# Optimization experiments

Hardware: AMD Instinct MI355X
Metric: run time of the kernel (lower is better)

## Reference

```python
import jax, jax.numpy as jnp
import numpy as np

B = 32
SIZES = [5023, 1256, 314, 79]
NS = [s + 1 for s in SIZES]   # padded vertex counts per level: [5024,1257,315,80]
K = 9
ENC_C = [3, 64, 128, 256]
DEC_C = [256, 128, 64, 3]
LATENT = 256


def _feast(x, nbr, wm, bm, wc, bc, act):
    # x: [B,N,F]; nbr: [N,K] int32 (col 0 = self index)
    xn = jnp.transpose(x[:, nbr, :], (0, 1, 3, 2))          # [B,N,F,K]
    xr = xn - xn[..., :1]                                    # relative to self neighbor
    logits = jnp.einsum('bnfk,of->bnok', xr, wm) + bm[None, None, :, None]  # conv1d(F->K,1)
    perm = jax.nn.softmax(logits, axis=2)                    # softmax over out-channel dim (torch dim=1)
    agg = jnp.einsum('bnfk,bnko->bnfo', xn, perm)            # [B,N,F,K] batched matmul
    Bv, N, F, Kv = agg.shape
    y = act(agg.reshape(Bv, N, F * Kv) @ wc.T + bc)          # linear(F*K -> out)
    mask = jnp.ones((N, 1), y.dtype).at[-1, 0].set(0.0)      # zero out padding vertex
    return y * mask


def _pool(x, L):
    # x: [B,M,F]; L: [Mp,M] -> [B,Mp,F]  (dense form of torch.spmm pooling)
    return jnp.einsum('pm,bmf->bpf', L, x)


def _forward(x, nbrs, Ds, Us, enc_p, dec_p, fce_w, fce_b, fcd_w, fcd_b):
    elu = jax.nn.elu
    ident = lambda v: v
    for i in range(3):
        wm, bm, wc, bc = enc_p[i]
        x = _feast(x, nbrs[i], wm, bm, wc, bc, elu)
        x = _pool(x, Ds[i])
    z = x.reshape(B, -1) @ fce_w.T + fce_b                    # [B, latent]
    x = (z @ fcd_w.T + fcd_b).reshape(B, NS[3], DEC_C[0])
    dec_nbrs = [nbrs[2], nbrs[1], nbrs[0]]
    dec_Us = [Us[2], Us[1], Us[0]]
    acts = [elu, elu, ident]                                  # last dconv uses identity
    for i in range(3):
        x = _pool(x, dec_Us[i])
        wm, bm, wc, bc = dec_p[i]
        x = _feast(x, dec_nbrs[i], wm, bm, wc, bc, acts[i])
    return x


def setup_inputs() -> dict:
    key = jax.random.key(0)
    ks = iter(jax.random.split(key, 64))
    nrm = lambda sh, s=0.05: jax.random.normal(next(ks), sh, dtype=jnp.float32) * s
    inp = {}
    inp['x'] = jax.random.normal(next(ks), (B, NS[0], 3), dtype=jnp.float32)
    for i in range(3):
        n = NS[i]
        nb = jax.random.randint(next(ks), (n, K), 0, n)
        nb = nb.at[:, 0].set(jnp.arange(n))
        inp[f'nbr{i}'] = nb.astype(jnp.int32)
    for i in range(3):
        cols = jax.random.randint(next(ks), (NS[i + 1],), 0, NS[i])
        inp[f'D{i}'] = jax.nn.one_hot(cols, NS[i], dtype=jnp.float32)   # sparse-like pooling
        cols_u = jax.random.randint(next(ks), (NS[i],), 0, NS[i + 1])
        inp[f'U{i}'] = jax.nn.one_hot(cols_u, NS[i + 1], dtype=jnp.float32)
    for i in range(3):
        fi, fo = ENC_C[i], ENC_C[i + 1]
        inp[f'e{i}_wm'] = nrm((K, fi)); inp[f'e{i}_bm'] = jnp.zeros((K,), jnp.float32)
        inp[f'e{i}_wc'] = nrm((fo, fi * K)); inp[f'e{i}_bc'] = jnp.zeros((fo,), jnp.float32)
    inp['fce_w'] = nrm((LATENT, NS[3] * ENC_C[3])); inp['fce_b'] = jnp.zeros((LATENT,), jnp.float32)
    inp['fcd_w'] = nrm((NS[3] * DEC_C[0], LATENT)); inp['fcd_b'] = jnp.zeros((NS[3] * DEC_C[0],), jnp.float32)
    for i in range(3):
        fi, fo = DEC_C[i], DEC_C[i + 1]
        inp[f'd{i}_wm'] = nrm((K, fi)); inp[f'd{i}_bm'] = jnp.zeros((K,), jnp.float32)
        inp[f'd{i}_wc'] = nrm((fo, fi * K)); inp[f'd{i}_bc'] = jnp.zeros((fo,), jnp.float32)
    return inp


def reference(x, nbr0, nbr1, nbr2, D0, D1, D2, U0, U1, U2,
              e0_wm, e0_bm, e0_wc, e0_bc, e1_wm, e1_bm, e1_wc, e1_bc,
              e2_wm, e2_bm, e2_wc, e2_bc, fce_w, fce_b, fcd_w, fcd_b,
              d0_wm, d0_bm, d0_wc, d0_bc, d1_wm, d1_bm, d1_wc, d1_bc,
              d2_wm, d2_bm, d2_wc, d2_bc):
    nbrs = [nbr0, nbr1, nbr2]
    Ds = [D0, D1, D2]
    Us = [U0, U1, U2]
    enc_p = [(e0_wm, e0_bm, e0_wc, e0_bc), (e1_wm, e1_bm, e1_wc, e1_bc), (e2_wm, e2_bm, e2_wc, e2_bc)]
    dec_p = [(d0_wm, d0_bm, d0_wc, d0_bc), (d1_wm, d1_bm, d1_wc, d1_bc), (d2_wm, d2_bm, d2_wc, d2_bc)]
    return _forward(x, nbrs, Ds, Us, enc_p, dec_p, fce_w, fce_b, fcd_w, fcd_b)
```

## Files before the change

### kernel.cpp

```cpp
#include <hip/hip_runtime.h>
#include <cstddef>

#define KN 9
typedef unsigned short u16;
typedef unsigned int u32;
typedef __attribute__((ext_vector_type(8))) short short8;
typedef __attribute__((ext_vector_type(4))) float f32x4;

__device__ inline u16 f2b(float f) {
    union { float f; u32 u; } v; v.f = f;
    u32 r = v.u + 0x7FFFu + ((v.u >> 16) & 1u);
    return (u16)(r >> 16);
}
__device__ inline float b2f(u16 h) {
    union { u32 u; float f; } v; v.u = ((u32)h) << 16; return v.f;
}

__device__ inline int xcd_swz(int bid, int n) {
    int q = n >> 3, r = n & 7;
    int x = bid & 7, pos = bid >> 3;
    return (x < r ? x * (q + 1) : r * (q + 1) + (x - r) * q) + pos;
}

__global__ void extract_idx_all(
    const float* __restrict__ D0, const float* __restrict__ D1, const float* __restrict__ D2,
    const float* __restrict__ U0, const float* __restrict__ U1, const float* __restrict__ U2,
    int* __restrict__ iD0, int* __restrict__ iD1, int* __restrict__ iD2,
    int* __restrict__ iU0, int* __restrict__ iU1, int* __restrict__ iU2)
{
    int blk = blockIdx.x;
    const float* L; int M; int* out; int p;
    if      (blk < 1257) { L = D0; M = 5024; out = iD0; p = blk; }
    else if (blk < 1572) { L = D1; M = 1257; out = iD1; p = blk - 1257; }
    else if (blk < 1652) { L = D2; M = 315;  out = iD2; p = blk - 1572; }
    else if (blk < 6676) { L = U0; M = 1257; out = iU0; p = blk - 1652; }
    else if (blk < 7933) { L = U1; M = 315;  out = iU1; p = blk - 6676; }
    else                 { L = U2; M = 80;   out = iU2; p = blk - 7933; }
    const float* row = L + (size_t)p * M;
    for (int m = threadIdx.x; m < M; m += 256)
        if (row[m] > 0.5f) out[p] = m;
}

__global__ void zero_f32(float4* __restrict__ p, int n4)
{
    int t = blockIdx.x * 256 + threadIdx.x;
    if (t < n4) p[t] = (float4){0.f, 0.f, 0.f, 0.f};
}

__device__ inline void wcr_one(const float* __restrict__ wc, u16* __restrict__ out, int t, int F) {
    int FK = F * KN;
    int c = t / FK, rem = t - c * FK, j = rem / F, f = rem - j * F;
    out[t] = f2b(wc[(size_t)c * FK + f * KN + j]);
}
__device__ inline void wg_one(const float* __restrict__ wc, u16* __restrict__ out, int t, int F, int C) {
    int n = t / F, f = t - n * F;
    int j = n / C, c = n - j * C;
    out[t] = f2b(wc[(size_t)c * (F * KN) + f * KN + j]);
}
__device__ inline void ccw_one(const float* __restrict__ wm, u16* __restrict__ out, int t, int F) {
    int n = t / F, f = t - n * F;
    out[t] = (n < KN) ? f2b(wm[n * F + f]) : (u16)0;
}
__global__ void cvt_weights(
    const float* __restrict__ e1_wc, const float* __restrict__ e2_wc,
    const float* __restrict__ d0_wc, const float* __restrict__ d1_wc,
    const float* __restrict__ e1_wm, const float* __restrict__ e2_wm,
    const float* __restrict__ d0_wm, const float* __restrict__ d1_wm,
    const float* __restrict__ d2_wm, const float* __restrict__ d2_wc,
    u16* __restrict__ wcrE1, u16* __restrict__ wcrE2,
    u16* __restrict__ wg0, u16* __restrict__ wg1,
    u16* __restrict__ ccwE1, u16* __restrict__ ccwE2,
    u16* __restrict__ ccwD0, u16* __restrict__ ccwD1,
    u16* __restrict__ w3, float* __restrict__ zbuf)
{
    int t = blockIdx.x * 256 + threadIdx.x;
    if (t < 73728)  { wcr_one(e1_wc, wcrE1, t, 64);       return; } t -= 73728;
    if (t < 294912) { wcr_one(e2_wc, wcrE2, t, 128);      return; } t -= 294912;
    if (t < 294912) { wg_one(d0_wc, wg0, t, 256, 128);    return; } t -= 294912;
    if (t < 73728)  { wg_one(d1_wc, wg1, t, 128, 64);     return; } t -= 73728;
    if (t < 4096)   { ccw_one(e1_wm, ccwE1, t, 64);       return; } t -= 4096;
    if (t < 8192)   { ccw_one(e2_wm, ccwE2, t, 128);      return; } t -= 8192;
    if (t < 16384)  { ccw_one(d0_wm, ccwD0, t, 256);      return; } t -= 16384;
    if (t < 8192)   { ccw_one(d1_wm, ccwD1, t, 128);      return; } t -= 8192;
    if (t < 4096) {
        int n = t >> 6, k = t & 63;
        float v = 0.f;
        if (n < KN) v = d2_wm[n * 64 + k];
        else if (n >= 9 && n < 36) {
            int cj = n - 9, j = cj / 3, c = cj - j * 3;
            v = d2_wc[(size_t)c * 576 + k * KN + j];
        }
        w3[t] = f2b(v);
        return;
    } t -= 4096;
    if (t < 8192) zbuf[t] = 0.f;
}

__global__ void compose_tables(
    const int* __restrict__ nbr0, const int* __restrict__ nbr1, const int* __restrict__ nbr2,
    const int* __restrict__ idxD1, const int* __restrict__ idxD2,
    const int* __restrict__ idxU0, const int* __restrict__ idxU1, const int* __restrict__ idxU2,
    int* __restrict__ nbrD1, int* __restrict__ nbrD2,
    int* __restrict__ nbrU2, int* __restrict__ nbrU1, int* __restrict__ nbrU0,
    int* __restrict__ maskE1, int* __restrict__ maskE2)
{
    int t = blockIdx.x * 256 + threadIdx.x;
    if (t < 2835)  { int p = t / 9, j = t - p * 9; nbrD1[p * 12 + j] = nbr1[idxD1[p] * 9 + j]; return; } t -= 2835;
    if (t < 720)   { int p = t / 9, j = t - p * 9; nbrD2[p * 12 + j] = nbr2[idxD2[p] * 9 + j]; return; } t -= 720;
    if (t < 2835)  { int p = t / 9, j = t - p * 9; nbrU2[p * 12 + j] = idxU2[nbr2[p * 9 + j]]; return; } t -= 2835;
    if (t < 11313) { int p = t / 9, j = t - p * 9; nbrU1[p * 12 + j] = idxU1[nbr1[p * 9 + j]]; return; } t -= 11313;
    if (t < 45216) { int p = t / 9, j = t - p * 9; nbrU0[p * 12 + j] = idxU0[nbr0[p * 9 + j]]; return; } t -= 45216;
    if (t < 315)   { maskE1[t] = (idxD1[t] == 1256) ? 1 : 0; return; } t -= 315;
    if (t < 80)    { maskE2[t] = (idxD2[t] == 314) ? 1 : 0; }
}

template<int NW, int OS>
__global__ __launch_bounds__(256) void cc_gemm(
    const u16* __restrict__ A, const u16* __restrict__ W,
    float* __restrict__ out, int M, int F)
{
    __shared__ u16 As[64 * 72];
    __shared__ u16 Ws[64 * 72];
    int tid = threadIdx.x;
    int mT = blockIdx.x * 64;
    int wid = tid >> 6, lane = tid & 63;
    int wr = wid >> 1, wcq = wid & 1;
    int r = lane & 15, g = lane >> 4;
    f32x4 acc[2][2];
    #pragma unroll
    for (int i = 0; i < 2; ++i)
        #pragma unroll
        for (int j = 0; j < 2; ++j)
            acc[i][j] = (f32x4){0.f, 0.f, 0.f, 0.f};

    for (int k0 = 0; k0 < F; k0 += 64) {
        #pragma unroll
        for (int h = 0; h < 2; ++h) {
            int gi = tid + h * 256;
            int m = gi >> 3, kg = gi & 7;
            uint4 va = {0u, 0u, 0u, 0u};
            int row = mT + m;
            if (row < M) va = *(const uint4*)(A + (size_t)row * F + k0 + kg * 8);
            *(uint4*)&As[m * 72 + kg * 8] = va;
            *(uint4*)&Ws[m * 72 + kg * 8] = *(const uint4*)(W + (size_t)m * F + k0 + kg * 8);
        }
        __syncthreads();
        #pragma unroll
        for (int S = 0; S < 2; ++S) {
            short8 af[2], bf[2];
            #pragma unroll
            for (int R = 0; R < 2; ++R)
                af[R] = *(const short8*)&As[(wr * 32 + R * 16 + r) * 72 + S * 32 + g * 8];
            #pragma unroll
            for (int C2 = 0; C2 < 2; ++C2)
                bf[C2] = *(const short8*)&Ws[(wcq * 32 + C2 * 16 + r) * 72 + S * 32 + g * 8];
            #pragma unroll
            for (int R = 0; R < 2; ++R)
                #pragma unroll
                for (int C2 = 0; C2 < 2; ++C2)
                    acc[R][C2] = __builtin_amdgcn_mfma_f32_16x16x32_bf16(af[R], bf[C2], acc[R][C2], 0, 0, 0);
        }
        __syncthreads();
    }
    #pragma unroll
    for (int R = 0; R < 2; ++R)
        #pragma unroll
        for (int C2 = 0; C2 < 2; ++C2)
            #pragma unroll
            for (int q = 0; q < 4; ++q) {
                int mm = mT + wr * 32 + R * 16 + g * 4 + q;
                int nn = wcq * 32 + C2 * 16 + r;
                if (mm < M && nn < NW)
                    out[(size_t)mm * OS + nn] = acc[R][C2][q];
            }
}

__global__ __launch_bounds__(256) void cc_gemmT(
    const u16* __restrict__ A, const u16* __restrict__ W,
    float* __restrict__ CCT, float* __restrict__ GWT, int M)
{
    __shared__ u16 As[64 * 72];
    __shared__ u16 Ws[64 * 72];
    int tid = threadIdx.x;
    int mT = blockIdx.x * 64;
    int wid = tid >> 6, lane = tid & 63;
    int wr = wid >> 1, wcq = wid & 1;
    int r = lane & 15, g = lane >> 4;
    f32x4 acc[2][2];
    #pragma unroll
    for (int i = 0; i < 2; ++i)
        #pragma unroll
        for (int j = 0; j < 2; ++j)
            acc[i][j] = (f32x4){0.f, 0.f, 0.f, 0.f};

    {
        #pragma unroll
        for (int h = 0; h < 2; ++h) {
            int gi = tid + h * 256;
            int m = gi >> 3, kg = gi & 7;
            uint4 va = {0u, 0u, 0u, 0u};
            int row = mT + m;
            if (row < M) va = *(const uint4*)(A + (size_t)row * 64 + kg * 8);
            *(uint4*)&As[m * 72 + kg * 8] = va;
            *(uint4*)&Ws[m * 72 + kg * 8] = *(const uint4*)(W + (size_t)m * 64 + kg * 8);
        }
        __syncthreads();
        #pragma unroll
        for (int S = 0; S < 2; ++S) {
            short8 af[2], bf[2];
            #pragma unroll
            for (int R = 0; R < 2; ++R)
                af[R] = *(const short8*)&As[(wr * 32 + R * 16 + r) * 72 + S * 32 + g * 8];
            #pragma unroll
            for (int C2 = 0; C2 < 2; ++C2)
                bf[C2] = *(const short8*)&Ws[(wcq * 32 + C2 * 16 + r) * 72 + S * 32 + g * 8];
            #pragma unroll
            for (int R = 0; R < 2; ++R)
                #pragma unroll
                for (int C2 = 0; C2 < 2; ++C2)
                    acc[R][C2] = __builtin_amdgcn_mfma_f32_16x16x32_bf16(af[R], bf[C2], acc[R][C2], 0, 0, 0);
        }
    }
    #pragma unroll
    for (int R = 0; R < 2; ++R)
        #pragma unroll
        for (int C2 = 0; C2 < 2; ++C2)
            #pragma unroll
            for (int q = 0; q < 4; ++q) {
                int mm = mT + wr * 32 + R * 16 + g * 4 + q;
                if (mm >= M) continue;
                int nn = wcq * 32 + C2 * 16 + r;
                if (nn >= 36) continue;
                int b = mm / 1257, p = mm - b * 1257;
                float val = acc[R][C2][q];
                if (nn < 9) {
                    CCT[((size_t)p * 9 + nn) * 32 + b] = val;
                } else {
                    int cj = nn - 9, j = cj / 3, c = cj - j * 3;
                    GWT[(size_t)p * 864 + j * 96 + b * 3 + c] = val;
                }
            }
}

template<int ACT, int MASK>
__global__ __launch_bounds__(256) void lin_gemm(
    const u16* __restrict__ A, const u16* __restrict__ W,
    const float* __restrict__ bias, u16* __restrict__ Y,
    const int* __restrict__ maskT,
    int M, int K, int N, int P)
{
    __shared__ u16 As[2][64 * 72];
    __shared__ u16 Ws[2][64 * 72];
    int tid = threadIdx.x;
    int mT = blockIdx.x * 64, nT = blockIdx.y * 64;
    int wid = tid >> 6, lane = tid & 63;
    int wr = wid >> 1, wcq = wid & 1;
    int r = lane & 15, g = lane >> 4;
    int lm = tid >> 3, lkg = tid & 7;
    f32x4 acc[2][2];
    #pragma unroll
    for (int i = 0; i < 2; ++i)
        #pragma unroll
        for (int j = 0; j < 2; ++j)
            acc[i][j] = (f32x4){0.f, 0.f, 0.f, 0.f};

    uint4 ra[2], rw[2];
    #pragma unroll
    for (int h = 0; h < 2; ++h) {
        int m = lm + h * 32;
        int row = mT + m;
        uint4 z; z.x = z.y = z.z = z.w = 0u;
        ra[h] = (row < M) ? *(const uint4*)(A + (size_t)row * K + lkg * 8) : z;
        rw[h] = *(const uint4*)(W + (size_t)(nT + m) * K + lkg * 8);
    }
    #pragma unroll
    for (int h = 0; h < 2; ++h) {
        int m = lm + h * 32;
        *(uint4*)&As[0][m * 72 + lkg * 8] = ra[h];
        *(uint4*)&Ws[0][m * 72 + lkg * 8] = rw[h];
    }

    int cur = 0;
    for (int k0 = 0; k0 < K; k0 += 64) {
        __syncthreads();
        bool more = (k0 + 64 < K);
        if (more) {
            int kn = k0 + 64;
            #pragma unroll
            for (int h = 0; h < 2; ++h) {
                int m = lm + h * 32;
                int row = mT + m;
                uint4 z; z.x = z.y = z.z = z.w = 0u;
                ra[h] = (row < M) ? *(const uint4*)(A + (size_t)row * K + kn + lkg * 8) : z;
                rw[h] = *(const uint4*)(W + (size_t)(nT + m) * K + kn + lkg * 8);
            }
        }
        #pragma unroll
        for (int S = 0; S < 2; ++S) {
            short8 af[2], bf[2];
            #pragma unroll
            for (int R = 0; R < 2; ++R)
                af[R] = *(const short8*)&As[cur][(wr * 32 + R * 16 + r) * 72 + S * 32 + g * 8];
            #pragma unroll
            for (int C2 = 0; C2 < 2; ++C2)
                bf[C2] = *(const short8*)&Ws[cur][(wcq * 32 + C2 * 16 + r) * 72 + S * 32 + g * 8];
            #pragma unroll
            for (int R = 0; R < 2; ++R)
                #pragma unroll
                for (int C2 = 0; C2 < 2; ++C2)
                    acc[R][C2] = __builtin_amdgcn_mfma_f32_16x16x32_bf16(af[R], bf[C2], acc[R][C2], 0, 0, 0);
        }
        if (more) {
            #pragma unroll
            for (int h = 0; h < 2; ++h) {
                int m = lm + h * 32;
                *(uint4*)&As[cur ^ 1][m * 72 + lkg * 8] = ra[h];
                *(uint4*)&Ws[cur ^ 1][m * 72 + lkg * 8] = rw[h];
            }
        }
        cur ^= 1;
    }

    #pragma unroll
    for (int R = 0; R < 2; ++R)
        #pragma unroll
        for (int C2 = 0; C2 < 2; ++C2)
            #pragma unroll
            for (int q = 0; q < 4; ++q) {
                int mm = mT + wr * 32 + R * 16 + g * 4 + q;
                if (mm >= M) continue;
                int nn = nT + wcq * 32 + C2 * 16 + r;
                float v = acc[R][C2][q];
                if (bias) v += bias[nn];
                if (ACT == 1) v = v > 0.f ? v : expm1f(v);
                if (MASK) { if (maskT[mm % P] != 0) v = 0.f; }
                Y[(size_t)mm * N + nn] = f2b(v);
            }
}

__global__ __launch_bounds__(256) void lin_gemm_sk(
    const u16* __restrict__ A, const u16* __restrict__ W,
    float* __restrict__ Yf, int M, int K, int N, int KSTEPS)
{
    __shared__ u16 As[64 * 72];
    __shared__ u16 Ws[64 * 72];
    int tid = threadIdx.x;
    int mT = blockIdx.x * 64, nT = blockIdx.y * 64;
    int kbase = blockIdx.z * KSTEPS * 64;
    int wid = tid >> 6, lane = tid & 63;
    int wr = wid >> 1, wcq = wid & 1;
    int r = lane & 15, g = lane >> 4;
    f32x4 acc[2][2];
    #pragma unroll
    for (int i = 0; i < 2; ++i)
        #pragma unroll
        for (int j = 0; j < 2; ++j)
            acc[i][j] = (f32x4){0.f, 0.f, 0.f, 0.f};

    for (int s = 0; s < KSTEPS; ++s) {
        int k0 = kbase + s * 64;
        #pragma unroll
        for (int h = 0; h < 2; ++h) {
            int gi = tid + h * 256;
            int m = gi >> 3, kg = gi & 7;
            uint4 va = {0u, 0u, 0u, 0u};
            int row = mT + m;
            if (row < M) va = *(const uint4*)(A + (size_t)row * K + k0 + kg * 8);
            *(uint4*)&As[m * 72 + kg * 8] = va;
            *(uint4*)&Ws[m * 72 + kg * 8] = *(const uint4*)(W + (size_t)(nT + m) * K + k0 + kg * 8);
        }
        __syncthreads();
        #pragma unroll
        for (int S = 0; S < 2; ++S) {
            short8 af[2], bf[2];
            #pragma unroll
            for (int R = 0; R < 2; ++R)
                af[R] = *(const short8*)&As[(wr * 32 + R * 16 + r) * 72 + S * 32 + g * 8];
            #pragma unroll
            for (int C2 = 0; C2 < 2; ++C2)
                bf[C2] = *(const short8*)&Ws[(wcq * 32 + C2 * 16 + r) * 72 + S * 32 + g * 8];
            #pragma unroll
            for (int R = 0; R < 2; ++R)
                #pragma unroll
                for (int C2 = 0; C2 < 2; ++C2)
                    acc[R][C2] = __builtin_amdgcn_mfma_f32_16x16x32_bf16(af[R], bf[C2], acc[R][C2], 0, 0, 0);
        }
        __syncthreads();
    }
    #pragma unroll
    for (int R = 0; R < 2; ++R)
        #pragma unroll
        for (int C2 = 0; C2 < 2; ++C2)
            #pragma unroll
            for (int q = 0; q < 4; ++q) {
                int mm = mT + wr * 32 + R * 16 + g * 4 + q;
                if (mm >= M) continue;
                int nn = nT + wcq * 32 + C2 * 16 + r;
                atomicAdd(&Yf[(size_t)mm * N + nn], acc[R][C2][q]);
            }
}

__global__ __launch_bounds__(256) void elu_mask_cvt(
    const float* __restrict__ Yf, const float* __restrict__ bias,
    const int* __restrict__ maskT, u16* __restrict__ Y,
    int M, int N, int P)
{
    int t = blockIdx.x * 256 + threadIdx.x;
    int tot = (M * N) >> 2;
    if (t >= tot) return;
    int e0 = t * 4;
    int m = e0 / N, n0 = e0 - m * N;
    float4 v = ((const float4*)Yf)[t];
    float o0 = v.x + bias[n0];
    float o1 = v.y + bias[n0 + 1];
    float o2 = v.z + bias[n0 + 2];
    float o3 = v.w + bias[n0 + 3];
    o0 = o0 > 0.f ? o0 : expm1f(o0);
    o1 = o1 > 0.f ? o1 : expm1f(o1);
    o2 = o2 > 0.f ? o2 : expm1f(o2);
    o3 = o3 > 0.f ? o3 : expm1f(o3);
    if (maskT[m % P] != 0) { o0 = 0.f; o1 = 0.f; o2 = 0.f; o3 = 0.f; }
    uint2 o;
    o.x = (u32)f2b(o0) | ((u32)f2b(o1) << 16);
    o.y = (u32)f2b(o2) | ((u32)f2b(o3) << 16);
    ((uint2*)Y)[t] = o;
}

__global__ __launch_bounds__(256) void fce_mfma(
    const u16* __restrict__ A, const float* __restrict__ Wf,
    const float* __restrict__ bias, float* __restrict__ z)
{
    __shared__ u16 As[32 * 72];
    __shared__ u16 Ws[64 * 72];
    int tid = threadIdx.x;
    int nT = blockIdx.x * 64;
    int kbase = blockIdx.y * 256;
    int wv = tid >> 6, lane = tid & 63;
    int r = lane & 15, g = lane >> 4;
    int m = tid >> 3, kg = tid & 7;
    f32x4 acc[2];
    acc[0] = (f32x4){0.f, 0.f, 0.f, 0.f};
    acc[1] = (f32x4){0.f, 0.f, 0.f, 0.f};

    for (int ks = 0; ks < 4; ++ks) {
        int k0 = kbase + ks * 64;
        *(uint4*)&As[m * 72 + kg * 8] = *(const uint4*)(A + (size_t)m * 20480 + k0 + kg * 8);
        #pragma unroll
        for (int h = 0; h < 2; ++h) {
            int row = m + h * 32;
            const float* wr2 = Wf + (size_t)(nT + row) * 20480 + k0 + kg * 8;
            float4 w0 = *(const float4*)(wr2);
            float4 w1 = *(const float4*)(wr2 + 4);
            u16 o[8] = { f2b(w0.x), f2b(w0.y), f2b(w0.z), f2b(w0.w),
                         f2b(w1.x), f2b(w1.y), f2b(w1.z), f2b(w1.w) };
            *(uint4*)&Ws[row * 72 + kg * 8] = *(const uint4*)o;
        }
        __syncthreads();
        #pragma unroll
        for (int S = 0; S < 2; ++S) {
            short8 bfr = *(const short8*)&Ws[(wv * 16 + r) * 72 + S * 32 + g * 8];
            #pragma unroll
            for (int R = 0; R < 2; ++R) {
                short8 af = *(const short8*)&As[(R * 16 + r) * 72 + S * 32 + g * 8];
                acc[R] = __builtin_amdgcn_mfma_f32_16x16x32_bf16(af, bfr, acc[R], 0, 0, 0);
            }
        }
        __syncthreads();
    }
    #pragma unroll
    for (int R = 0; R < 2; ++R)
        #pragma unroll
        for (int q = 0; q < 4; ++q) {
            int mm = R * 16 + g * 4 + q;
            int nn = nT + wv * 16 + r;
            float v = acc[R][q];
            if (blockIdx.y == 0) v += bias[nn];
            atomicAdd(&z[mm * 256 + nn], v);
        }
}

__global__ __launch_bounds__(256) void fcd_mfma(
    const float* __restrict__ Af, const float* __restrict__ Wf,
    const float* __restrict__ bias, u16* __restrict__ Y)
{
    __shared__ u16 As[64 * 72];
    __shared__ u16 Ws[64 * 72];
    int tid = threadIdx.x;
    int nT = blockIdx.x * 64;
    int wid = tid >> 6, lane = tid & 63;
    int wr = wid >> 1, wcq = wid & 1;
    int r = lane & 15, g = lane >> 4;
    int m = tid >> 3, kg = tid & 7;
    f32x4 acc[2][2];
    #pragma unroll
    for (int i = 0; i < 2; ++i)
        #pragma unroll
        for (int j = 0; j < 2; ++j)
            acc[i][j] = (f32x4){0.f, 0.f, 0.f, 0.f};

    for (int k0 = 0; k0 < 256; k0 += 64) {
        {
            const float* ar = Af + (size_t)m * 256 + k0 + kg * 8;
            float4 a0 = *(const float4*)(ar);
            float4 a1 = *(const float4*)(ar + 4);
            u16 o[8] = { f2b(a0.x), f2b(a0.y), f2b(a0.z), f2b(a0.w),
                         f2b(a1.x), f2b(a1.y), f2b(a1.z), f2b(a1.w) };
            *(uint4*)&As[m * 72 + kg * 8] = *(const uint4*)o;
            uint4 z4; z4.x = z4.y = z4.z = z4.w = 0u;
            *(uint4*)&As[(m + 32) * 72 + kg * 8] = z4;
        }
        #pragma unroll
        for (int h = 0; h < 2; ++h) {
            int row = m + h * 32;
            const float* wr2 = Wf + (size_t)(nT + row) * 256 + k0 + kg * 8;
            float4 w0 = *(const float4*)(wr2);
            float4 w1 = *(const float4*)(wr2 + 4);
            u16 o[8] = { f2b(w0.x), f2b(w0.y), f2b(w0.z), f2b(w0.w),
                         f2b(w1.x), f2b(w1.y), f2b(w1.z), f2b(w1.w) };
            *(uint4*)&Ws[row * 72 + kg * 8] = *(const uint4*)o;
        }
        __syncthreads();
        #pragma unroll
        for (int S = 0; S < 2; ++S) {
            short8 af[2], bf[2];
            #pragma unroll
            for (int R = 0; R < 2; ++R)
                af[R] = *(const short8*)&As[(wr * 32 + R * 16 + r) * 72 + S * 32 + g * 8];
            #pragma unroll
            for (int C2 = 0; C2 < 2; ++C2)
                bf[C2] = *(const short8*)&Ws[(wcq * 32 + C2 * 16 + r) * 72 + S * 32 + g * 8];
            #pragma unroll
            for (int R = 0; R < 2; ++R)
                #pragma unroll
                for (int C2 = 0; C2 < 2; ++C2)
                    acc[R][C2] = __builtin_amdgcn_mfma_f32_16x16x32_bf16(af[R], bf[C2], acc[R][C2], 0, 0, 0);
        }
        __syncthreads();
    }
    #pragma unroll
    for (int R = 0; R < 2; ++R)
        #pragma unroll
        for (int C2 = 0; C2 < 2; ++C2)
            #pragma unroll
            for (int q = 0; q < 4; ++q) {
                int mm = wr * 32 + R * 16 + g * 4 + q;
                if (mm >= 32) continue;
                int nn = nT + wcq * 32 + C2 * 16 + r;
                float v = acc[R][C2][q] + bias[nn];
                Y[(size_t)mm * 20480 + nn] = f2b(v);
            }
}

template<int F>
__global__ __launch_bounds__(256) void feast_agg(
    const u16* __restrict__ x, const float* __restrict__ cc,
    const int* __restrict__ nbrT, const float* __restrict__ bm,
    u16* __restrict__ agg, int Pin, int P, int Mtot)
{
    constexpr int FC = F / 64;
    __shared__ float s_p[4][81];
    __shared__ int s_nb[4][KN];
    int tid = threadIdx.x, wid = tid >> 6, lane = tid & 63;
    int row = xcd_swz(blockIdx.x, gridDim.x) * 4 + wid;
    bool aw = row < Mtot;
    int b = 0, p = 0;
    if (aw) { b = row / P; p = row - b * P; }
    if (aw && lane < KN) s_nb[wid][lane] = b * Pin + nbrT[p * 12 + lane];
    __syncthreads();

    if (aw && lane < KN) {
        int j = lane;
        const float* c0 = cc + (size_t)s_nb[wid][0] * 16;
        const float* cj = cc + (size_t)s_nb[wid][j] * 16;
        float L[KN];
        #pragma unroll
        for (int i = 0; i < KN; ++i) L[i] = bm[i] + cj[i] - c0[i];
        float mx = L[0];
        #pragma unroll
        for (int i = 1; i < KN; ++i) mx = fmaxf(mx, L[i]);
        float s = 0.f;
        #pragma unroll
        for (int i = 0; i < KN; ++i) { L[i] = __expf(L[i] - mx); s += L[i]; }
        float inv = 1.f / s;
        #pragma unroll
        for (int i = 0; i < KN; ++i) s_p[wid][i * KN + j] = L[i] * inv;
    }
    __syncthreads();

    if (aw) {
        float xn[KN][FC];
        #pragma unroll
        for (int i = 0; i < KN; ++i) {
            const u16* xr = x + (size_t)s_nb[wid][i] * F;
            #pragma unroll
            for (int c = 0; c < FC; ++c) xn[i][c] = b2f(xr[lane + c * 64]);
        }
        #pragma unroll
        for (int j = 0; j < KN; ++j) {
            float a[FC];
            #pragma unroll
            for (int c = 0; c < FC; ++c) a[c] = 0.f;
            #pragma unroll
            for (int i = 0; i < KN; ++i) {
                float pv = s_p[wid][i * KN + j];
                #pragma unroll
                for (int c = 0; c < FC; ++c) a[c] += xn[i][c] * pv;
            }
            u16* orow = agg + (size_t)row * (KN * F) + j * F;
            #pragma unroll
            for (int c = 0; c < FC; ++c) orow[lane + c * 64] = f2b(a[c]);
        }
    }
}

template<int C>
__global__ __launch_bounds__(256) void mix_feast(
    const u16* __restrict__ G, const float* __restrict__ cc,
    const int* __restrict__ nbrT, const float* __restrict__ bm,
    const float* __restrict__ bc, u16* __restrict__ y,
    int Pin, int P, int Mtot)
{
    constexpr int GS = KN * C;
    constexpr int CC_ = C / 64;
    __shared__ float s_p[4][81];
    __shared__ int s_nb[4][KN];
    int tid = threadIdx.x, wid = tid >> 6, lane = tid & 63;
    int row = xcd_swz(blockIdx.x, gridDim.x) * 4 + wid;
    bool aw = row < Mtot;
    int b = 0, p = 0;
    if (aw) { b = row / P; p = row - b * P; }
    if (aw && lane < KN) s_nb[wid][lane] = b * Pin + nbrT[p * 12 + lane];
    __syncthreads();

    if (aw && lane < KN) {
        int j = lane;
        const float* c0 = cc + (size_t)s_nb[wid][0] * 16;
        const float* cj = cc + (size_t)s_nb[wid][j] * 16;
        float L[KN];
        #pragma unroll
        for (int i = 0; i < KN; ++i) L[i] = bm[i] + cj[i] - c0[i];
        float mx = L[0];
        #pragma unroll
        for (int i = 1; i < KN; ++i) mx = fmaxf(mx, L[i]);
        float s = 0.f;
        #pragma unroll
        for (int i = 0; i < KN; ++i) { L[i] = __expf(L[i] - mx); s += L[i]; }
        float inv = 1.f / s;
        #pragma unroll
        for (int i = 0; i < KN; ++i) s_p[wid][i * KN + j] = L[i] * inv;
    }
    __syncthreads();

    if (aw) {
        float acc[CC_];
        #pragma unroll
        for (int c = 0; c < CC_; ++c) acc[c] = bc[lane + c * 64];
        #pragma unroll
        for (int i = 0; i < KN; ++i) {
            const u16* gr = G + (size_t)s_nb[wid][i] * GS;
            float pv[KN];
            #pragma unroll
            for (int j = 0; j < KN; ++j) pv[j] = s_p[wid][i * KN + j];
            #pragma unroll
            for (int j = 0; j < KN; ++j)
                #pragma unroll
                for (int c = 0; c < CC_; ++c)
                    acc[c] += pv[j] * b2f(gr[j * C + lane + c * 64]);
        }
        #pragma unroll
        for (int c = 0; c < CC_; ++c) {
            float v = acc[c];
            v = v > 0.f ? v : expm1f(v);
            if (p == P - 1) v = 0.f;
            y[(size_t)row * C + lane + c * 64] = f2b(v);
        }
    }
}

__global__ __launch_bounds__(256) void feast_e0(
    const float* __restrict__ x, const int* __restrict__ nbr,
    const int* __restrict__ sel,
    const float* __restrict__ wm, const float* __restrict__ bm,
    const float* __restrict__ wcw, const float* __restrict__ bc,
    u16* __restrict__ y,
    int Nin, int P, int Nlevel, int Mtot)
{
    constexpr int F = 3, C = 64, FS = 4, Q = 27;
    __shared__ float s_wm[KN * FS];
    __shared__ float s_wc[C * Q];
    __shared__ float s_bm[KN];
    __shared__ float s_xn[4][KN * FS];
    __shared__ float s_lg[4][81];
    __shared__ float s_pm[4][81];
    __shared__ float s_ag[4][Q];
    __shared__ int   s_idx[4][KN];

    int tid = threadIdx.x, wid = tid >> 6, lane = tid & 63;
    for (int t = tid; t < KN * F; t += 256) { int i = t / F, f = t - i * F; s_wm[i * FS + f] = wm[t]; }
    for (int t = tid; t < C * Q; t += 256) s_wc[t] = wcw[t];
    if (tid < KN) s_bm[tid] = bm[tid];

    int wg = xcd_swz(blockIdx.x, gridDim.x) * 4 + wid;
    bool aw = wg < Mtot;
    int b = 0, p = 0, n = 0;
    if (aw) {
        b = wg / P; p = wg - b * P;
        n = sel[p];
    }
    if (aw && lane < KN) s_idx[wid][lane] = nbr[n * KN + lane];
    __syncthreads();

    if (aw) {
        const float* xb = x + (size_t)b * Nin * F;
        for (int t = lane; t < KN * F; t += 64) {
            int i = t / F, f = t - i * F;
            s_xn[wid][i * FS + f] = xb[(size_t)s_idx[wid][i] * F + f];
        }
    }
    __syncthreads();

    if (aw) {
        for (int pr = lane; pr < 81; pr += 64) {
            int i = pr / KN, j = pr - i * KN;
            float acc = s_bm[i];
            for (int f = 0; f < F; ++f)
                acc += (s_xn[wid][j * FS + f] - s_xn[wid][f]) * s_wm[i * FS + f];
            s_lg[wid][pr] = acc;
        }
    }
    __syncthreads();

    if (aw && lane < KN) {
        int j = lane;
        float mx = -1e30f;
        #pragma unroll
        for (int i = 0; i < KN; ++i) mx = fmaxf(mx, s_lg[wid][i * KN + j]);
        float sm = 0.f, ev[KN];
        #pragma unroll
        for (int i = 0; i < KN; ++i) { ev[i] = __expf(s_lg[wid][i * KN + j] - mx); sm += ev[i]; }
        float inv = 1.f / sm;
        #pragma unroll
        for (int i = 0; i < KN; ++i) s_pm[wid][i * KN + j] = ev[i] * inv;
    }
    __syncthreads();

    if (aw) {
        for (int t = lane; t < Q; t += 64) {
            int f = t / KN, j = t - f * KN;
            float acc = 0.f;
            #pragma unroll
            for (int i = 0; i < KN; ++i) acc += s_xn[wid][i * FS + f] * s_pm[wid][i * KN + j];
            s_ag[wid][t] = acc;
        }
    }
    __syncthreads();

    if (aw) {
        int c = lane;
        float acc = 0.f;
        #pragma unroll
        for (int q = 0; q < Q; ++q)
            acc += s_wc[c * Q + q] * s_ag[wid][q];
        float val = acc + bc[c];
        val = val > 0.f ? val : expm1f(val);
        if (n == Nlevel - 1) val = 0.f;
        y[(size_t)wg * C + c] = f2b(val);
    }
}

__global__ __launch_bounds__(256) void mix_d2t(
    const float* __restrict__ CCT, const float* __restrict__ GWT,
    const int* __restrict__ nbrT,
    const float* __restrict__ bm9, const float* __restrict__ bc3,
    float* __restrict__ out)
{
    __shared__ float s_out[8][32][3];
    int tid = threadIdx.x, wid = tid >> 6, lane = tid & 63;
    int sub = lane >> 5, b = lane & 31;
    int vbase = xcd_swz(blockIdx.x, gridDim.x) * 8;
    int v = vbase + wid * 2 + sub;

    int nbi[KN];
    #pragma unroll
    for (int i = 0; i < KN; ++i) nbi[i] = nbrT[v * 12 + i];
    float bmr[KN];
    #pragma unroll
    for (int i = 0; i < KN; ++i) bmr[i] = bm9[i];

    float cc0[KN];
    {
        const float* c0 = CCT + (size_t)nbi[0] * 9 * 32 + b;
        #pragma unroll
        for (int f = 0; f < KN; ++f) cc0[f] = c0[f * 32];
    }
    float a0 = bc3[0], a1 = bc3[1], a2 = bc3[2];
    #pragma unroll
    for (int j = 0; j < KN; ++j) {
        const float* cj = CCT + (size_t)nbi[j] * 9 * 32 + b;
        float L[KN];
        #pragma unroll
        for (int i = 0; i < KN; ++i) L[i] = bmr[i] + cj[i * 32] - cc0[i];
        float mx = L[0];
        #pragma unroll
        for (int i = 1; i < KN; ++i) mx = fmaxf(mx, L[i]);
        float sm = 0.f;
        #pragma unroll
        for (int i = 0; i < KN; ++i) { L[i] = __expf(L[i] - mx); sm += L[i]; }
        float inv = 1.f / sm;
        #pragma unroll
        for (int i = 0; i < KN; ++i) {
            float pv = L[i] * inv;
            const float* g = GWT + (size_t)nbi[i] * 864 + j * 96 + b * 3;
            a0 += pv * g[0];
            a1 += pv * g[1];
            a2 += pv * g[2];
        }
    }
    if (v == 5023) { a0 = 0.f; a1 = 0.f; a2 = 0.f; }
    s_out[wid * 2 + sub][b][0] = a0;
    s_out[wid * 2 + sub][b][1] = a1;
    s_out[wid * 2 + sub][b][2] = a2;
    __syncthreads();
    {
        int bb = tid >> 3, vi = tid & 7;
        float* dst = out + ((size_t)bb * 5024 + vbase + vi) * 3;
        dst[0] = s_out[vi][bb][0];
        dst[1] = s_out[vi][bb][1];
        dst[2] = s_out[vi][bb][2];
    }
}

extern "C" void kernel_launch(void* const* d_in, const int* in_sizes, int n_in,
                              void* d_out, int out_size, void* d_ws, size_t ws_size,
                              hipStream_t stream)
{
    const float* x     = (const float*)d_in[0];
    const int*   nbr0  = (const int*)d_in[1];
    const int*   nbr1  = (const int*)d_in[2];
    const int*   nbr2  = (const int*)d_in[3];
    const float* D0    = (const float*)d_in[4];
    const float* U0    = (const float*)d_in[5];
    const float* D1    = (const float*)d_in[6];
    const float* U1    = (const float*)d_in[7];
    const float* D2    = (const float*)d_in[8];
    const float* U2    = (const float*)d_in[9];
    const float* e0_wm = (const float*)d_in[10]; const float* e0_bm = (const float*)d_in[11];
    const float* e0_wc = (const float*)d_in[12]; const float* e0_bc = (const float*)d_in[13];
    const float* e1_wm = (const float*)d_in[14]; const float* e1_bm = (const float*)d_in[15];
    const float* e1_wc = (const float*)d_in[16]; const float* e1_bc = (const float*)d_in[17];
    const float* e2_wm = (const float*)d_in[18]; const float* e2_bm = (const float*)d_in[19];
    const float* e2_wc = (const float*)d_in[20]; const float* e2_bc = (const float*)d_in[21];
    const float* fce_w = (const float*)d_in[22]; const float* fce_b = (const float*)d_in[23];
    const float* fcd_w = (const float*)d_in[24]; const float* fcd_b = (const float*)d_in[25];
    const float* d0_wm = (const float*)d_in[26]; const float* d0_bm = (const float*)d_in[27];
    const float* d0_wc = (const float*)d_in[28]; const float* d0_bc = (const float*)d_in[29];
    const float* d1_wm = (const float*)d_in[30]; const float* d1_bm = (const float*)d_in[31];
    const float* d1_wc = (const float*)d_in[32]; const float* d1_bc = (const float*)d_in[33];
    const float* d2_wm = (const float*)d_in[34]; const float* d2_bm = (const float*)d_in[35];
    const float* d2_wc = (const float*)d_in[36]; const float* d2_bc = (const float*)d_in[37];

    char* w = (char*)d_ws;
    int* idxD0 = (int*)(w);
    int* idxD1 = idxD0 + 1257;
    int* idxD2 = idxD1 + 315;
    int* idxU0 = idxD2 + 80;
    int* idxU1 = idxU0 + 5024;
    int* idxU2 = idxU1 + 1257;
    int* nbrD1  = (int*)(w + 33024);
    int* nbrD2  = (int*)(w + 48144);
    int* nbrU2  = (int*)(w + 51984);
    int* nbrU1  = (int*)(w + 67104);
    int* nbrU0  = (int*)(w + 127440);
    int* maskE1 = (int*)(w + 368640);
    int* maskE2 = (int*)(w + 369920);
    u16* wcrE1 = (u16*)(w + 370432);
    u16* wcrE2 = (u16*)(w + 517888);
    u16* wg0   = (u16*)(w + 1107712);
    u16* wg1   = (u16*)(w + 1697536);
    u16* ccwE1 = (u16*)(w + 1844992);
    u16* ccwE2 = (u16*)(w + 1853184);
    u16* ccwD0 = (u16*)(w + 1869568);
    u16* ccwD1 = (u16*)(w + 1902336);
    u16* w3    = (u16*)(w + 1918720);
    float* zbuf = (float*)(w + 1926912);

    u16*   X1   = (u16*)  (w + 2097152);
    float* CC1  = (float*)(w + 7245824);
    u16*   AGG1 = (u16*)  (w + 9820160);
    u16*   X2   = (u16*)  (w + 21432320);
    float* CC2  = (float*)(w + 24012800);
    u16*   AGG2 = (u16*)  (w + 24657920);
    u16*   X3   = (u16*)  (w + 2097152);
    u16*   X3P  = (u16*)  (w + 3407872);
    float* CCD0 = (float*)(w + 4718592);
    u16*   G0   = (u16*)  (w + 4882432);
    u16*   XD1P = (u16*)  (w + 10780672);
    float* CCD1 = (float*)(w + 13361152);
    u16*   G1   = (u16*)  (w + 14006272);
    u16*   XD2P = (u16*)  (w + 25618432);
    float* CCT  = (float*)(w + 30767104);
    float* GWT  = (float*)(w + 32215168);
    float* X2F  = (float*)(w + 36559360);
    float* X3F  = (float*)(w + 41720320);

    extract_idx_all<<<8248, 256, 0, stream>>>(D0, D1, D2, U0, U1, U2,
                                              idxD0, idxD1, idxD2, idxU0, idxU1, idxU2);
    cvt_weights<<<3072, 256, 0, stream>>>(e1_wc, e2_wc, d0_wc, d1_wc,
                                          e1_wm, e2_wm, d0_wm, d1_wm, d2_wm, d2_wc,
                                          wcrE1, wcrE2, wg0, wg1,
                                          ccwE1, ccwE2, ccwD0, ccwD1, w3, zbuf);
    compose_tables<<<248, 256, 0, stream>>>(nbr0, nbr1, nbr2,
                                            idxD1, idxD2, idxU0, idxU1, idxU2,
                                            nbrD1, nbrD2, nbrU2, nbrU1, nbrU0,
                                            maskE1, maskE2);
    zero_f32<<<1900, 256, 0, stream>>>((float4*)X2F, 486400);

    feast_e0<<<10056, 256, 0, stream>>>(x, nbr0, idxD0, e0_wm, e0_bm, e0_wc, e0_bc,
                                        X1, 5024, 1257, 5024, 40224);
    cc_gemm<16, 16><<<629, 256, 0, stream>>>(X1, ccwE1, CC1, 40224, 64);
    feast_agg<64><<<2520, 256, 0, stream>>>(X1, CC1, nbrD1, e1_bm, AGG1, 1257, 315, 10080);
    lin_gemm_sk<<<dim3(158, 2, 3), 256, 0, stream>>>(AGG1, wcrE1, X2F, 10080, 576, 128, 3);
    elu_mask_cvt<<<1260, 256, 0, stream>>>(X2F, e1_bc, maskE1, X2, 10080, 128, 315);
    cc_gemm<16, 16><<<158, 256, 0, stream>>>(X2, ccwE2, CC2, 10080, 128);
    feast_agg<128><<<640, 256, 0, stream>>>(X2, CC2, nbrD2, e2_bm, AGG2, 315, 80, 2560);
    lin_gemm_sk<<<dim3(40, 4, 6), 256, 0, stream>>>(AGG2, wcrE2, X3F, 2560, 1152, 256, 3);
    elu_mask_cvt<<<640, 256, 0, stream>>>(X3F, e2_bc, maskE2, X3, 2560, 256, 80);

    fce_mfma<<<dim3(4, 80), 256, 0, stream>>>(X3, fce_w, fce_b, zbuf);
    fcd_mfma<<<320, 256, 0, stream>>>(zbuf, fcd_w, fcd_b, X3P);

    cc_gemm<16, 16><<<40, 256, 0, stream>>>(X3P, ccwD0, CCD0, 2560, 256);
    lin_gemm<0, 0><<<dim3(40, 18), 256, 0, stream>>>(X3P, wg0, nullptr, G0, nullptr,
                                                     2560, 256, 1152, 1);
    mix_feast<128><<<2520, 256, 0, stream>>>(G0, CCD0, nbrU2, d0_bm, d0_bc, XD1P,
                                             80, 315, 10080);
    cc_gemm<16, 16><<<158, 256, 0, stream>>>(XD1P, ccwD1, CCD1, 10080, 128);
    lin_gemm<0, 0><<<dim3(158, 9), 256, 0, stream>>>(XD1P, wg1, nullptr, G1, nullptr,
                                                     10080, 128, 576, 1);
    mix_feast<64><<<10056, 256, 0, stream>>>(G1, CCD1, nbrU1, d1_bm, d1_bc, XD2P,
                                             315, 1257, 40224);
    cc_gemmT<<<629, 256, 0, stream>>>(XD2P, w3, CCT, GWT, 40224);
    mix_d2t<<<628, 256, 0, stream>>>(CCT, GWT, nbrU0, d2_bm, d2_bc, (float*)d_out);
}
```

Before: 256.1 us.

## Pack multiple rows per wave in decoder mix kernel with 16-byte loads

Measured after the change: 345.6 us. 1.35x slower.

```diff
diff --git a/kernel.cpp b/kernel.cpp
--- a/kernel.cpp
+++ b/kernel.cpp
@@ -614,66 +614,102 @@
 }
 
 template<int C>
-__global__ __launch_bounds__(256) void mix_feast(
+__global__ __launch_bounds__(256) void mix_feast_v(
     const u16* __restrict__ G, const float* __restrict__ cc,
     const int* __restrict__ nbrT, const float* __restrict__ bm,
     const float* __restrict__ bc, u16* __restrict__ y,
     int Pin, int P, int Mtot)
 {
+    constexpr int LPR = C / 8;
+    constexpr int RPW = 64 / LPR;
+    constexpr int RPB = 4 * RPW;
     constexpr int GS = KN * C;
-    constexpr int CC_ = C / 64;
-    __shared__ float s_p[4][81];
-    __shared__ int s_nb[4][KN];
+    __shared__ float s_p[RPB][84];
+    __shared__ int   s_nb[RPB][KN];
+
     int tid = threadIdx.x, wid = tid >> 6, lane = tid & 63;
-    int row = xcd_swz(blockIdx.x, gridDim.x) * 4 + wid;
-    bool aw = row < Mtot;
-    int b = 0, p = 0;
-    if (aw) { b = row / P; p = row - b * P; }
-    if (aw && lane < KN) s_nb[wid][lane] = b * Pin + nbrT[p * 12 + lane];
+    int rowbase = xcd_swz(blockIdx.x, gridDim.x) * RPB;
+
+    for (int t = tid; t < RPB * KN; t += 256) {
+        int rr = t / KN, j = t - rr * KN;
+        int row = rowbase + rr;
+        int v = 0;
+        if (row < Mtot) {
+            int b = row / P, p = row - b * P;
+            v = b * Pin + nbrT[p * 12 + j];
+        }
+        s_nb[rr][j] = v;
+    }
     __syncthreads();
 
-    if (aw && lane < KN) {
-        int j = lane;
-        const float* c0 = cc + (size_t)s_nb[wid][0] * 16;
-        const float* cj = cc + (size_t)s_nb[wid][j] * 16;
-        float L[KN];
-        #pragma unroll
-        for (int i = 0; i < KN; ++i) L[i] = bm[i] + cj[i] - c0[i];
-        float mx = L[0];
-        #pragma unroll
-        for (int i = 1; i < KN; ++i) mx = fmaxf(mx, L[i]);
-        float s = 0.f;
-        #pragma unroll
-        for (int i = 0; i < KN; ++i) { L[i] = __expf(L[i] - mx); s += L[i]; }
-        float inv = 1.f / s;
-        #pragma unroll
-        for (int i = 0; i < KN; ++i) s_p[wid][i * KN + j] = L[i] * inv;
+    {
+        int rl, j0;
+        if (C == 64) { rl = wid * RPW + (lane >> 3); j0 = lane & 7; }
+        else         { rl = wid * RPW + (lane >> 4); j0 = lane & 15; }
+        int row = rowbase + rl;
+        if (row < Mtot && j0 <= KN) {
+            float cc0[KN], bmr[KN];
+            const float* c0 = cc + (size_t)s_nb[rl][0] * 16;
+            #pragma unroll
+            for (int i = 0; i < KN; ++i) { cc0[i] = c0[i]; bmr[i] = bm[i]; }
+            int nj = 1;
+            int jl[2]; jl[0] = j0; jl[1] = -1;
+            if (C == 64 && j0 == 0) { jl[1] = 8; nj = 2; }
+            if (j0 >= KN) nj = 0;
+            for (int t = 0; t < nj; ++t) {
+                int j = jl[t];
+                const float* cj = cc + (size_t)s_nb[rl][j] * 16;
+                float L[KN];
+                #pragma unroll
+                for (int i = 0; i < KN; ++i) L[i] = bmr[i] + cj[i] - cc0[i];
+                float mx = L[0];
+                #pragma unroll
+                for (int i = 1; i < KN; ++i) mx = fmaxf(mx, L[i]);
+                float sm = 0.f;
+                #pragma unroll
+                for (int i = 0; i < KN; ++i) { L[i] = __expf(L[i] - mx); sm += L[i]; }
+                float inv = 1.f / sm;
+                #pragma unroll
+                for (int i = 0; i < KN; ++i) s_p[rl][i * KN + j] = L[i] * inv;
+            }
+        }
     }
     __syncthreads();
 
-    if (aw) {
-        float acc[CC_];
-        #pragma unroll
-        for (int c = 0; c < CC_; ++c) acc[c] = bc[lane + c * 64];
+    {
+        int rl = wid * RPW + lane / LPR;
+        int coff = (lane % LPR) * 8;
+        int row = rowbase + rl;
+        if (row >= Mtot) return;
+        int b = row / P, p = row - b * P;
+        (void)b;
+        float acc[8];
+        #pragma unroll
+        for (int k = 0; k < 8; ++k) acc[k] = bc[coff + k];
         #pragma unroll
         for (int i = 0; i < KN; ++i) {
-            const u16* gr = G + (size_t)s_nb[wid][i] * GS;
+            const u16* gr = G + (size_t)s_nb[rl][i] * GS + coff;
             float pv[KN];
             #pragma unroll
-            for (int j = 0; j < KN; ++j) pv[j] = s_p[wid][i * KN + j];
-            #pragma unroll
-            for (int j = 0; j < KN; ++j)
-                #pragma unroll
-                for (int c = 0; c < CC_; ++c)
-                    acc[c] += pv[j] * b2f(gr[j * C + lane + c * 64]);
-        }
-        #pragma unroll
-        for (int c = 0; c < CC_; ++c) {
-            float v = acc[c];
+            for (int j = 0; j < KN; ++j) pv[j] = s_p[rl][i * KN + j];
+            #pragma unroll
+            for (int j = 0; j < KN; ++j) {
+                uint4 gv = *(const uint4*)(gr + j * C);
+                const u16* ge = (const u16*)&gv;
+                float p0 = pv[j];
+                #pragma unroll
+                for (int k = 0; k < 8; ++k) acc[k] += p0 * b2f(ge[k]);
+            }
+        }
+        u16 o[8];
+        #pragma unroll
+        for (int k = 0; k < 8; ++k) {
+            float v = acc[k];
             v = v > 0.f ? v : expm1f(v);
             if (p == P - 1) v = 0.f;
-            y[(size_t)row * C + lane + c * 64] = f2b(v);
-        }
+            o[k] = f2b(v);
+        }
+        *(uint4*)(y + (size_t)row * C + coff) = *(const uint4*)o;
     }
 }
 
@@ -932,13 +968,13 @@
     cc_gemm<16, 16><<<40, 256, 0, stream>>>(X3P, ccwD0, CCD0, 2560, 256);
     lin_gemm<0, 0><<<dim3(40, 18), 256, 0, stream>>>(X3P, wg0, nullptr, G0, nullptr,
                                                      2560, 256, 1152, 1);
-    mix_feast<128><<<2520, 256, 0, stream>>>(G0, CCD0, nbrU2, d0_bm, d0_bc, XD1P,
-                                             80, 315, 10080);
+    mix_feast_v<128><<<630, 256, 0, stream>>>(G0, CCD0, nbrU2, d0_bm, d0_bc, XD1P,
+                                              80, 315, 10080);
     cc_gemm<16, 16><<<158, 256, 0, stream>>>(XD1P, ccwD1, CCD1, 10080, 128);
     lin_gemm<0, 0><<<dim3(158, 9), 256, 0, stream>>>(XD1P, wg1, nullptr, G1, nullptr,
                                                      10080, 128, 576, 1);
-    mix_feast<64><<<10056, 256, 0, stream>>>(G1, CCD1, nbrU1, d1_bm, d1_bc, XD2P,
-                                             315, 1257, 40224);
+    mix_feast_v<64><<<1257, 256, 0, stream>>>(G1, CCD1, nbrU1, d1_bm, d1_bc, XD2P,
+                                              315, 1257, 40224);
     cc_gemmT<<<629, 256, 0, stream>>>(XD2P, w3, CCT, GWT, 40224);
     mix_d2t<<<628, 256, 0, stream>>>(CCT, GWT, nbrU0, d2_bm, d2_bc, (float*)d_out);
 }
```
